# Kernel tuning notes

Measured on AMD Instinct MI355X. Metric: run time of the kernel, lower is better.

## Reference

```python
import jax, jax.numpy as jnp
import numpy as np

B, S, D_IN, D_H = 16, 4096, 512, 512

def setup_inputs() -> dict:
    key = jax.random.key(0)
    ks = jax.random.split(key, 8)
    inp = {
        "input": jax.random.normal(ks[0], (B, D_IN), dtype=jnp.float32),
        "context": jax.random.normal(ks[1], (B, S, D_IN), dtype=jnp.float32),
        "mask": jax.random.bernoulli(ks[2], 0.2, (B, S)),
        # parameters (torch nn.Linear layout: W [out,in], b [out])
        "W_in": jax.random.normal(ks[3], (D_H, D_IN), dtype=jnp.float32) / np.sqrt(D_IN),
        "b_in": jax.random.normal(ks[4], (D_H,), dtype=jnp.float32) * 0.01,
        "W_ctx": jax.random.normal(ks[5], (D_H, D_IN), dtype=jnp.float32) / np.sqrt(D_IN),
        "b_ctx": jax.random.normal(ks[6], (D_H,), dtype=jnp.float32) * 0.01,
        "v": jax.random.normal(ks[7], (D_H,), dtype=jnp.float32),
    }
    return inp


def reference(input, context, mask, W_in, b_in, W_ctx, b_ctx, v):
    # inp: [B, H] projected decoder state
    inp = input @ W_in.T + b_in
    # ctx: [B, S, H] projected context (this is what the torch code matmuls
    # with the softmax weights, i.e. hidden lives in hidden_dim space)
    ctx = context @ W_ctx.T + b_ctx
    # additive (Bahdanau) scores: v . tanh(inp + ctx) -> [B, S]
    scores = jnp.einsum("h,bsh->bs", v, jnp.tanh(inp[:, None, :] + ctx))
    # masked positions get -inf so they receive zero softmax weight
    scores = jnp.where(mask, -jnp.inf, scores)
    attn = jax.nn.softmax(scores, axis=-1)  # [B, S]
    # weighted sum of projected context: [B, H]
    hidden = jnp.einsum("bsh,bs->bh", ctx, attn)
    return hidden, attn
```

## Files before the change

kernel.cpp:

```cpp
#include <hip/hip_runtime.h>
#include <hip/hip_bf16.h>

#define B_  16
#define S_  4096
#define DIN 512
#define DH  512

typedef _Float16 f16x8 __attribute__((ext_vector_type(8)));
typedef float    f32x4 __attribute__((ext_vector_type(4)));


__device__ __forceinline__ float fast_tanh(float x) {
    float e = __expf(2.f * x);
    return 1.f - 2.f * __builtin_amdgcn_rcpf(e + 1.f);
}

__device__ __forceinline__ void gload_lds16(const void* g, void* l) {
    __builtin_amdgcn_global_load_lds(
        (const __attribute__((address_space(1))) void*)g,
        (__attribute__((address_space(3))) void*)l, 16, 0, 0);
}

__global__ void prep_kernel(const float* __restrict__ input,
                            const float* __restrict__ W_in,
                            const float* __restrict__ b_in,
                            const float* __restrict__ W_ctx,
                            const float* __restrict__ b_ctx,
                            const void*  __restrict__ mask,
                            _Float16* __restrict__ W16,
                            float* __restrict__ addv,
                            int* __restrict__ maskflag) {
    int blk = blockIdx.x;
    int tid = threadIdx.x;
    if (blk < 256) {
        int base = blk * 1024 + tid * 4;
        float4 wv = *(const float4*)(W_ctx + base);
        union { _Float16 f[4]; ushort4 u; } cv;
        cv.f[0] = (_Float16)wv.x; cv.f[1] = (_Float16)wv.y;
        cv.f[2] = (_Float16)wv.z; cv.f[3] = (_Float16)wv.w;
        *(ushort4*)(W16 + base) = cv.u;
    } else if (blk < 288) {
        int t = blk - 256;
        int b = t >> 1;
        int h = ((t & 1) << 8) + tid;
        __shared__ float inrow[DIN];
        inrow[tid]       = input[b * DIN + tid];
        inrow[tid + 256] = input[b * DIN + tid + 256];
        __syncthreads();
        const float* wr = W_in + (size_t)h * DIN;
        float acc = 0.f;
        for (int k = 0; k < DIN; k += 4) {
            float4 w4 = *(const float4*)(wr + k);
            acc += w4.x * inrow[k] + w4.y * inrow[k + 1]
                 + w4.z * inrow[k + 2] + w4.w * inrow[k + 3];
        }
        addv[b * DH + h] = acc + b_in[h] + b_ctx[h];
    } else {
        const uint4* m4 = (const uint4*)mask;
        unsigned int orw = 0;
#pragma unroll
        for (int it = 0; it < 16; ++it) {
            uint4 w = m4[it * 256 + tid];
            orw |= (w.x | w.y | w.z | w.w);
        }
        int found = ((orw & 0xFFFFFF00u) != 0) ? 1 : 0;
        __shared__ int f;
        if (tid == 0) f = 0;
        __syncthreads();
        if (found) atomicOr(&f, 1);
        __syncthreads();
        if (tid == 0) maskflag[0] = f;
    }
}


__global__ __launch_bounds__(256, 2)
void score_kernel(const float* __restrict__ context,
                  const _Float16* __restrict__ W16,
                  const float* __restrict__ addv,
                  const float* __restrict__ v,
                  const void* __restrict__ mask,
                  const int* __restrict__ maskflag,
                  float* __restrict__ scores) {
    __shared__ _Float16 Bs[2][16384];

    const int tid  = threadIdx.x;
    const int wave = tid >> 6;
    const int lane = tid & 63;
    const int l15  = lane & 15;
    const int q    = lane >> 4;
    const int b    = blockIdx.x >> 5;
    const int s0   = (blockIdx.x & 31) * 128;

    f16x8 a[2][16];
#pragma unroll
    for (int t = 0; t < 2; ++t) {
        const float* arow = context +
            ((size_t)b * S_ + s0 + wave * 32 + t * 16 + l15) * DIN + q * 8;
#pragma unroll
        for (int kc = 0; kc < 16; ++kc) {
            float4 x0 = *(const float4*)(arow + kc * 32);
            float4 x1 = *(const float4*)(arow + kc * 32 + 4);
            f16x8 tt;
            tt[0] = (_Float16)x0.x; tt[1] = (_Float16)x0.y;
            tt[2] = (_Float16)x0.z; tt[3] = (_Float16)x0.w;
            tt[4] = (_Float16)x1.x; tt[5] = (_Float16)x1.y;
            tt[6] = (_Float16)x1.z; tt[7] = (_Float16)x1.w;
            a[t][kc] = tt;
        }
    }

    const float* avb = addv + b * DH;
    float rowsum[2][4] = {{0.f,0.f,0.f,0.f},{0.f,0.f,0.f,0.f}};

#define STAGE_CHUNK(c_)                                                        \
    {                                                                          \
        int win_s = (c_) >> 1, kh_s = (c_) & 1;                                \
        _Float16* dst = &Bs[(c_) & 1][0];                                      \
        _Pragma("unroll")                                                      \
        for (int u = 0; u < 8; ++u) {                                          \
            int id = wave * 8 + u;                                             \
            int kl = id >> 2, j = id & 3;                                      \
            const _Float16* g = W16 +                                          \
                (size_t)(win_s * 64 + j * 16 + l15) * DIN +                    \
                kh_s * 256 + kl * 32 + q * 8;                                  \
            gload_lds16(g, dst + id * 512);                                    \
        }                                                                      \
    }

    STAGE_CHUNK(0);

    for (int win = 0; win < 8; ++win) {
        f32x4 acc[2][4];
#pragma unroll
        for (int t = 0; t < 2; ++t)
#pragma unroll
            for (int j = 0; j < 4; ++j) acc[t][j] = (f32x4){0.f,0.f,0.f,0.f};

#pragma unroll
        for (int kh = 0; kh < 2; ++kh) {
            int c = win * 2 + kh;
            __syncthreads();
            if (c + 1 < 16) STAGE_CHUNK(c + 1);
            const _Float16* Bbuf = &Bs[c & 1][0];
#pragma unroll
            for (int kl = 0; kl < 8; ++kl) {
                int kc = kh * 8 + kl;
                f16x8 bf0 = *(const f16x8*)&Bbuf[(kl * 4 + 0) * 512 + q * 128 + l15 * 8];
                f16x8 bf1 = *(const f16x8*)&Bbuf[(kl * 4 + 1) * 512 + q * 128 + l15 * 8];
                f16x8 bf2 = *(const f16x8*)&Bbuf[(kl * 4 + 2) * 512 + q * 128 + l15 * 8];
                f16x8 bf3 = *(const f16x8*)&Bbuf[(kl * 4 + 3) * 512 + q * 128 + l15 * 8];
                acc[0][0] = __builtin_amdgcn_mfma_f32_16x16x32_f16(a[0][kc], bf0, acc[0][0], 0, 0, 0);
                acc[1][0] = __builtin_amdgcn_mfma_f32_16x16x32_f16(a[1][kc], bf0, acc[1][0], 0, 0, 0);
                acc[0][1] = __builtin_amdgcn_mfma_f32_16x16x32_f16(a[0][kc], bf1, acc[0][1], 0, 0, 0);
                acc[1][1] = __builtin_amdgcn_mfma_f32_16x16x32_f16(a[1][kc], bf1, acc[1][1], 0, 0, 0);
                acc[0][2] = __builtin_amdgcn_mfma_f32_16x16x32_f16(a[0][kc], bf2, acc[0][2], 0, 0, 0);
                acc[1][2] = __builtin_amdgcn_mfma_f32_16x16x32_f16(a[1][kc], bf2, acc[1][2], 0, 0, 0);
                acc[0][3] = __builtin_amdgcn_mfma_f32_16x16x32_f16(a[0][kc], bf3, acc[0][3], 0, 0, 0);
                acc[1][3] = __builtin_amdgcn_mfma_f32_16x16x32_f16(a[1][kc], bf3, acc[1][3], 0, 0, 0);
            }
        }
#pragma unroll
        for (int j = 0; j < 4; ++j) {
            int n = win * 64 + j * 16 + l15;
            float av = avb[n];
            float vv = v[n];
#pragma unroll
            for (int t = 0; t < 2; ++t)
#pragma unroll
                for (int r = 0; r < 4; ++r)
                    rowsum[t][r] += vv * fast_tanh(acc[t][j][r] + av);
        }
    }

    int isByte = maskflag[0];
#pragma unroll
    for (int t = 0; t < 2; ++t)
#pragma unroll
        for (int r = 0; r < 4; ++r) {
            float s = rowsum[t][r];
            s += __shfl_xor(s, 1, 16);
            s += __shfl_xor(s, 2, 16);
            s += __shfl_xor(s, 4, 16);
            s += __shfl_xor(s, 8, 16);
            if (l15 == 0) {
                int srow = s0 + wave * 32 + t * 16 + q * 4 + r;
                int idx = b * S_ + srow;
                int msk = isByte ? (int)((const unsigned char*)mask)[idx]
                                 : ((const int*)mask)[idx];
                scores[idx] = msk ? -__builtin_inff() : s;
            }
        }
}

__global__ __launch_bounds__(256)
void final_kernel(const float* __restrict__ scores,
                  const float* __restrict__ context,
                  const float* __restrict__ W_ctx,
                  const float* __restrict__ b_ctx,
                  float* __restrict__ attn,
                  float* __restrict__ hidden) {
    __shared__ float rbuf[4];
    __shared__ float wsumS[DIN];
    __shared__ int   selIdx[S_];
    __shared__ float selW[S_];
    __shared__ int   selCount;

    int b = blockIdx.x, tid = threadIdx.x;
    int wv = tid >> 6, ln = tid & 63;
    const float* sr = scores + b * S_;

    float mx = -__builtin_inff();
    for (int s = tid; s < S_; s += 256) mx = fmaxf(mx, sr[s]);
    for (int o = 1; o < 64; o <<= 1) mx = fmaxf(mx, __shfl_xor(mx, o, 64));
    if (ln == 0) rbuf[wv] = mx;
    __syncthreads();
    mx = fmaxf(fmaxf(rbuf[0], rbuf[1]), fmaxf(rbuf[2], rbuf[3]));
    __syncthreads();

    float sum = 0.f;
    for (int s = tid; s < S_; s += 256) sum += __expf(sr[s] - mx);
    for (int o = 1; o < 64; o <<= 1) sum += __shfl_xor(sum, o, 64);
    if (ln == 0) rbuf[wv] = sum;
    if (tid == 0) selCount = 0;
    __syncthreads();
    sum = rbuf[0] + rbuf[1] + rbuf[2] + rbuf[3];
    float inv = 1.f / sum;

    float* ab = attn + b * S_;
    for (int s = tid; s < S_; s += 256) {
        float p = __expf(sr[s] - mx) * inv;
        ab[s] = p;
        if (p > 1e-9f) {
            int k = atomicAdd(&selCount, 1);
            selIdx[k] = s;
            selW[k]  = p;
        }
    }
    __syncthreads();

    int cnt = selCount;
    float acc0 = 0.f, acc1 = 0.f;
    for (int i = 0; i < cnt; ++i) {
        int s = selIdx[i];
        float w = selW[i];
        const float* cr = context + ((size_t)b * S_ + s) * DIN;
        acc0 += w * cr[tid];
        acc1 += w * cr[tid + 256];
    }
    wsumS[tid]       = acc0;
    wsumS[tid + 256] = acc1;
    __syncthreads();

#pragma unroll
    for (int hh = 0; hh < 2; ++hh) {
        int h = tid + hh * 256;
        const float* wr = W_ctx + (size_t)h * DIN;
        float acc = 0.f;
        for (int k = 0; k < DIN; k += 4) {
            float4 w4 = *(const float4*)(wr + k);
            acc += w4.x * wsumS[k] + w4.y * wsumS[k + 1]
                 + w4.z * wsumS[k + 2] + w4.w * wsumS[k + 3];
        }
        hidden[b * DH + h] = acc + b_ctx[h];
    }
}

extern "C" void kernel_launch(void* const* d_in, const int* in_sizes, int n_in,
                              void* d_out, int out_size, void* d_ws, size_t ws_size,
                              hipStream_t stream) {
    const float* input   = (const float*)d_in[0];
    const float* context = (const float*)d_in[1];
    const void*  mask    = d_in[2];
    const float* W_in    = (const float*)d_in[3];
    const float* b_in    = (const float*)d_in[4];
    const float* W_ctx   = (const float*)d_in[5];
    const float* b_ctx   = (const float*)d_in[6];
    const float* v       = (const float*)d_in[7];

    char* ws = (char*)d_ws;
    _Float16* W16   = (_Float16*)ws;
    float* addv     = (float*)(ws + 524288);
    float* scores   = (float*)(ws + 557056);
    int*   maskflag = (int*)(ws + 851968);

    float* hidden = (float*)d_out;
    float* attn   = (float*)d_out + B_ * DH;

    prep_kernel<<<289, 256, 0, stream>>>(input, W_in, b_in, W_ctx, b_ctx, mask,
                                         W16, addv, maskflag);
    score_kernel<<<512, 256, 0, stream>>>(context, W16, addv, v,
                                          mask, maskflag, scores);
    final_kernel<<<B_, 256, 0, stream>>>(scores, context, W_ctx, b_ctx,
                                         attn, hidden);
}
```

Baseline: 317.1 us.

## Double score-kernel block size to share W tiles, cache bias/v in LDS, unroll gather

The score kernel now uses 512-thread blocks that each cover 256 sequence rows, with half as many blocks. Each staged W16 tile is therefore reused by twice as many waves, and each wave issues half the LDS staging loads. The addv and v vectors are copied into shared memory once per block, and the final kernel's sparse weighted context gather is unrolled by four with independent accumulators to expose more memory-level parallelism. In exchange, a 512-thread block with 32 f16x8 A fragments per thread raises register pressure and may lower occupancy. The grid of 256 blocks may also leave part of the GPU underfilled.

```diff
diff --git a/kernel.cpp b/kernel.cpp
--- a/kernel.cpp
+++ b/kernel.cpp
@@ -74,7 +74,7 @@
 }
 
 
-__global__ __launch_bounds__(256, 2)
+__global__ __launch_bounds__(512, 2)
 void score_kernel(const float* __restrict__ context,
                   const _Float16* __restrict__ W16,
                   const float* __restrict__ addv,
@@ -83,14 +83,19 @@
                   const int* __restrict__ maskflag,
                   float* __restrict__ scores) {
     __shared__ _Float16 Bs[2][16384];
+    __shared__ float avS[DH];
+    __shared__ float vvS[DH];
 
     const int tid  = threadIdx.x;
     const int wave = tid >> 6;
     const int lane = tid & 63;
     const int l15  = lane & 15;
     const int q    = lane >> 4;
-    const int b    = blockIdx.x >> 5;
-    const int s0   = (blockIdx.x & 31) * 128;
+    const int b    = blockIdx.x >> 4;
+    const int s0   = (blockIdx.x & 15) * 256;
+
+    avS[tid] = addv[b * DH + tid];
+    vvS[tid] = v[tid];
 
     f16x8 a[2][16];
 #pragma unroll
@@ -110,7 +115,6 @@
         }
     }
 
-    const float* avb = addv + b * DH;
     float rowsum[2][4] = {{0.f,0.f,0.f,0.f},{0.f,0.f,0.f,0.f}};
 
 #define STAGE_CHUNK(c_)                                                        \
@@ -118,8 +122,8 @@
         int win_s = (c_) >> 1, kh_s = (c_) & 1;                                \
         _Float16* dst = &Bs[(c_) & 1][0];                                      \
         _Pragma("unroll")                                                      \
-        for (int u = 0; u < 8; ++u) {                                          \
-            int id = wave * 8 + u;                                             \
+        for (int u = 0; u < 4; ++u) {                                          \
+            int id = wave * 4 + u;                                             \
             int kl = id >> 2, j = id & 3;                                      \
             const _Float16* g = W16 +                                          \
                 (size_t)(win_s * 64 + j * 16 + l15) * DIN +                    \
@@ -163,8 +167,8 @@
 #pragma unroll
         for (int j = 0; j < 4; ++j) {
             int n = win * 64 + j * 16 + l15;
-            float av = avb[n];
-            float vv = v[n];
+            float av = avS[n];
+            float vv = vvS[n];
 #pragma unroll
             for (int t = 0; t < 2; ++t)
 #pragma unroll
@@ -240,11 +244,31 @@
     __syncthreads();
 
     int cnt = selCount;
-    float acc0 = 0.f, acc1 = 0.f;
-    for (int i = 0; i < cnt; ++i) {
+    const float* cb = context + (size_t)b * S_ * DIN;
+    float a00 = 0.f, a01 = 0.f, a10 = 0.f, a11 = 0.f;
+    float a20 = 0.f, a21 = 0.f, a30 = 0.f, a31 = 0.f;
+    int i = 0;
+    for (; i + 4 <= cnt; i += 4) {
+        const float* c0 = cb + (size_t)selIdx[i]     * DIN;
+        const float* c1 = cb + (size_t)selIdx[i + 1] * DIN;
+        const float* c2 = cb + (size_t)selIdx[i + 2] * DIN;
+        const float* c3 = cb + (size_t)selIdx[i + 3] * DIN;
+        float w0 = selW[i], w1 = selW[i + 1], w2 = selW[i + 2], w3 = selW[i + 3];
+        float x00 = c0[tid], x01 = c0[tid + 256];
+        float x10 = c1[tid], x11 = c1[tid + 256];
+        float x20 = c2[tid], x21 = c2[tid + 256];
+        float x30 = c3[tid], x31 = c3[tid + 256];
+        a00 += w0 * x00; a01 += w0 * x01;
+        a10 += w1 * x10; a11 += w1 * x11;
+        a20 += w2 * x20; a21 += w2 * x21;
+        a30 += w3 * x30; a31 += w3 * x31;
+    }
+    float acc0 = (a00 + a10) + (a20 + a30);
+    float acc1 = (a01 + a11) + (a21 + a31);
+    for (; i < cnt; ++i) {
         int s = selIdx[i];
         float w = selW[i];
-        const float* cr = context + ((size_t)b * S_ + s) * DIN;
+        const float* cr = cb + (size_t)s * DIN;
         acc0 += w * cr[tid];
         acc1 += w * cr[tid + 256];
     }
@@ -289,7 +313,7 @@
 
     prep_kernel<<<289, 256, 0, stream>>>(input, W_in, b_in, W_ctx, b_ctx, mask,
                                          W16, addv, maskflag);
-    score_kernel<<<512, 256, 0, stream>>>(context, W16, addv, v,
+    score_kernel<<<256, 512, 0, stream>>>(context, W16, addv, v,
                                           mask, maskflag, scores);
     final_kernel<<<B_, 256, 0, stream>>>(scores, context, W_ctx, b_ctx,
                                          attn, hidden);
```

Result: no change. 318.9 us (+0.6%).
